# Kernel tuning notes

Hardware: AMD Instinct MI355X
Metric: run time of the kernel (lower is better)

## Reference

```python
import jax, jax.numpy as jnp
import numpy as np

EMBED_DIM = 1024
NUM_HEADS = 16
HEAD_DIM = EMBED_DIM // NUM_HEADS


def setup_inputs() -> dict:
    key = jax.random.key(0)
    ks = jax.random.split(key, 9)
    s = 1.0 / np.sqrt(EMBED_DIM)
    x = jax.random.normal(ks[0], (2, 2048, EMBED_DIM), dtype=jnp.float32)
    # nn.Linear weights are [out, in]; store transposed [in, out] for x @ W
    Wq = jax.random.uniform(ks[1], (EMBED_DIM, EMBED_DIM), jnp.float32, -s, s)
    bq = jax.random.uniform(ks[2], (EMBED_DIM,), jnp.float32, -s, s)
    Wk = jax.random.uniform(ks[3], (EMBED_DIM, EMBED_DIM), jnp.float32, -s, s)
    bk = jax.random.uniform(ks[4], (EMBED_DIM,), jnp.float32, -s, s)
    Wv = jax.random.uniform(ks[5], (EMBED_DIM, EMBED_DIM), jnp.float32, -s, s)
    bv = jax.random.uniform(ks[6], (EMBED_DIM,), jnp.float32, -s, s)
    Wo = jax.random.uniform(ks[7], (EMBED_DIM, EMBED_DIM), jnp.float32, -s, s)
    bo = jax.random.uniform(ks[8], (EMBED_DIM,), jnp.float32, -s, s)
    return {"x": x, "Wq": Wq, "bq": bq, "Wk": Wk, "bk": bk,
            "Wv": Wv, "bv": bv, "Wo": Wo, "bo": bo}


def reference(x, Wq, bq, Wk, bk, Wv, bv, Wo, bo):
    B, N, C = x.shape
    H, D = NUM_HEADS, HEAD_DIM
    scale = 1.0 / np.sqrt(D).astype(np.float32)
    # project and split heads: [B, H, N, D]
    q = (x @ Wq + bq).reshape(B, N, H, D).transpose(0, 2, 1, 3)
    k = (x @ Wk + bk).reshape(B, N, H, D).transpose(0, 2, 1, 3)
    v = (x @ Wv + bv).reshape(B, N, H, D).transpose(0, 2, 1, 3)
    scores = jnp.einsum('bhnd,bhmd->bhnm', q, k) * scale  # [B,H,N,N]
    probs = jax.nn.softmax(scores, axis=-1)
    attn = jnp.einsum('bhnm,bhmd->bhnd', probs, v)  # [B,H,N,D]
    attn = attn.transpose(0, 2, 1, 3).reshape(B, N, C)
    return attn @ Wo + bo
```

## Files before the change

### kernel.cpp

```cpp
#include <hip/hip_runtime.h>
#include <hip/hip_bf16.h>
#include <stdint.h>


#define DEVI __device__ __forceinline__

typedef __attribute__((ext_vector_type(8))) short bf16x8;
typedef __attribute__((ext_vector_type(4))) float f32x4;
typedef __attribute__((ext_vector_type(16))) float f32x16;

#define Z16 ((f32x16){0.f,0.f,0.f,0.f,0.f,0.f,0.f,0.f,0.f,0.f,0.f,0.f,0.f,0.f,0.f,0.f})

DEVI unsigned short f2bf(float f) {
  union { float f; uint32_t u; } v; v.f = f;
  uint32_t u = v.u;
  u += 0x7FFFu + ((u >> 16) & 1u);
  return (unsigned short)(u >> 16);
}

DEVI uint32_t cvtpk_bf16(float lo, float hi) {
  uint32_t r;
  asm("v_cvt_pk_bf16_f32 %0, %1, %2" : "=v"(r) : "v"(lo), "v"(hi));
  return r;
}

DEVI void pl32swap(uint32_t& a, uint32_t& b) {
  asm volatile("v_permlane32_swap_b32 %0, %1" : "+v"(a), "+v"(b));
}

DEVI float fexp2(float x) {
#if __has_builtin(__builtin_amdgcn_exp2f)
  return __builtin_amdgcn_exp2f(x);
#else
  return exp2f(x);
#endif
}

typedef __attribute__((address_space(3))) uint32_t lds_u32_t;
typedef const __attribute__((address_space(1))) uint32_t glb_u32_t;

DEVI void gl2lds16(const void* g, void* l) {
  __builtin_amdgcn_global_load_lds((glb_u32_t*)g, (lds_u32_t*)l, 16, 0, 0);
}

#define MFMA16(a, b, c) __builtin_amdgcn_mfma_f32_16x16x32_bf16((a), (b), (c), 0, 0, 0)
#define MFMA3216(a, b, c) __builtin_amdgcn_mfma_f32_32x32x16_bf16((a), (b), (c), 0, 0, 0)

__global__ void prep_k(const float* __restrict__ x, unsigned short* __restrict__ xb,
                       const float* __restrict__ w0, const float* __restrict__ w1,
                       const float* __restrict__ w2, const float* __restrict__ w3,
                       unsigned short* __restrict__ o0, unsigned short* __restrict__ o1,
                       unsigned short* __restrict__ o2, unsigned short* __restrict__ o3) {
  __shared__ float tile[32][33];
  const int z = blockIdx.z;
  if (z >= 4) {
    int i = ((z - 4) * 1024 + blockIdx.y * 32 + blockIdx.x) * 256 + threadIdx.x;
    float4 a = ((const float4*)x)[i * 2];
    float4 b = ((const float4*)x)[i * 2 + 1];
    union { unsigned short s[8]; uint4 v; } u;
    u.s[0] = f2bf(a.x); u.s[1] = f2bf(a.y); u.s[2] = f2bf(a.z); u.s[3] = f2bf(a.w);
    u.s[4] = f2bf(b.x); u.s[5] = f2bf(b.y); u.s[6] = f2bf(b.z); u.s[7] = f2bf(b.w);
    ((uint4*)xb)[i] = u.v;
    return;
  }
  const float* in = (z == 0) ? w0 : (z == 1) ? w1 : (z == 2) ? w2 : w3;
  unsigned short* out = (z == 0) ? o0 : (z == 1) ? o1 : (z == 2) ? o2 : o3;
  int bx = blockIdx.x * 32, by = blockIdx.y * 32;
  int tx = threadIdx.x & 31, ty = threadIdx.x >> 5;
#pragma unroll
  for (int i = 0; i < 32; i += 8)
    tile[ty + i][tx] = in[(size_t)(by + ty + i) * 1024 + bx + tx];
  __syncthreads();
#pragma unroll
  for (int i = 0; i < 32; i += 8)
    out[(size_t)(bx + ty + i) * 1024 + by + tx] = f2bf(tile[tx][ty + i]);
}

__global__ __launch_bounds__(256, 2)
void gemm_qkv(const unsigned short* __restrict__ A, const unsigned short* __restrict__ Bt,
              const float* __restrict__ bq, const float* __restrict__ bk,
              const float* __restrict__ bv,
              unsigned short* __restrict__ Qb, unsigned short* __restrict__ Kb,
              unsigned short* __restrict__ Vtb) {
  __shared__ unsigned short lA[2][128 * 32];
  __shared__ unsigned short lB[2][128 * 32];
  const int t = threadIdx.x;
  const int mbase = blockIdx.y * 128, nbase = blockIdx.x * 128;
  const int wv = t >> 6, lane = t & 63, lr = lane & 15, lg = lane >> 4;
  const int wr = wv >> 1, wc = wv & 1;
  const int K = 1024;
  const int c0 = t, c1 = t + 256;

#define GSTAGE(buf, k0)                                                                     \
  do {                                                                                      \
    gl2lds16(A + ((size_t)(mbase + (c0 >> 2)) * K + (k0) + (c0 & 3) * 8), &lA[buf][c0 * 8]);\
    gl2lds16(Bt + ((size_t)(nbase + (c0 >> 2)) * K + (k0) + (c0 & 3) * 8), &lB[buf][c0 * 8]);\
    gl2lds16(A + ((size_t)(mbase + (c1 >> 2)) * K + (k0) + (c1 & 3) * 8), &lA[buf][c1 * 8]);\
    gl2lds16(Bt + ((size_t)(nbase + (c1 >> 2)) * K + (k0) + (c1 & 3) * 8), &lB[buf][c1 * 8]);\
  } while (0)

  f32x4 acc[4][4];
#pragma unroll
  for (int i = 0; i < 4; i++)
#pragma unroll
    for (int j = 0; j < 4; j++) acc[i][j] = (f32x4){0.f, 0.f, 0.f, 0.f};

  GSTAGE(0, 0);
  int buf = 0;
  for (int kk = 0; kk < 32; ++kk) {
    if (kk < 31) {
      GSTAGE(buf ^ 1, (kk + 1) * 32);
      asm volatile("s_waitcnt vmcnt(4)");
    } else {
      asm volatile("s_waitcnt vmcnt(0)");
    }
    __builtin_amdgcn_s_barrier();
    __builtin_amdgcn_sched_barrier(0);
    bf16x8 af[4], bfr[4];
#pragma unroll
    for (int i = 0; i < 4; i++)
      af[i] = *(const bf16x8*)&lA[buf][(wr * 64 + i * 16 + lr) * 32 + lg * 8];
#pragma unroll
    for (int j = 0; j < 4; j++)
      bfr[j] = *(const bf16x8*)&lB[buf][(wc * 64 + j * 16 + lr) * 32 + lg * 8];
    __builtin_amdgcn_s_setprio(1);
#pragma unroll
    for (int i = 0; i < 4; i++)
#pragma unroll
      for (int j = 0; j < 4; j++)
        acc[i][j] = MFMA16(af[i], bfr[j], acc[i][j]);
    __builtin_amdgcn_s_setprio(0);
    __builtin_amdgcn_s_barrier();
    buf ^= 1;
  }
#undef GSTAGE

#pragma unroll
  for (int i = 0; i < 4; i++) {
#pragma unroll
    for (int j = 0; j < 4; j++) {
#pragma unroll
      for (int r = 0; r < 4; r++) {
        int grow = mbase + wr * 64 + i * 16 + lg * 4 + r;
        int gcol = nbase + wc * 64 + j * 16 + lr;
        float v = acc[i][j][r];
        if (gcol < 1024) {
          Qb[(size_t)grow * 1024 + gcol] = f2bf((v + bq[gcol]) * 0.18033688011f);
        } else if (gcol < 2048) {
          int c2 = gcol - 1024;
          Kb[(size_t)grow * 1024 + c2] = f2bf(v + bk[c2]);
        } else {
          int vc = gcol - 2048, hh = vc >> 6, d = vc & 63;
          int bb = grow >> 11, np = grow & 2047;
          Vtb[((size_t)((bb * 16 + hh) * 64 + d) << 11) + np] = f2bf(v + bv[vc]);
        }
      }
    }
  }
}

__global__ __launch_bounds__(256, 2)
void gemm_out(const unsigned short* __restrict__ A, const unsigned short* __restrict__ Bt,
              const float* __restrict__ bias, float* __restrict__ outp) {
  __shared__ unsigned short lA[2][128 * 32];
  __shared__ unsigned short lB[2][64 * 32];
  const int t = threadIdx.x;
  const int mbase = blockIdx.y * 128, nbase = blockIdx.x * 64;
  const int wv = t >> 6, lane = t & 63, lr = lane & 15, lg = lane >> 4;
  const int wr = wv >> 1, wc = wv & 1;
  const int K = 1024, N = 1024;
  const int a0 = t, a1 = t + 256;
  const int bg = t;

#define GSTAGE(buf, k0)                                                                     \
  do {                                                                                      \
    gl2lds16(A + ((size_t)(mbase + (a0 >> 2)) * K + (k0) + (a0 & 3) * 8), &lA[buf][a0 * 8]);\
    gl2lds16(A + ((size_t)(mbase + (a1 >> 2)) * K + (k0) + (a1 & 3) * 8), &lA[buf][a1 * 8]);\
    gl2lds16(Bt + ((size_t)(nbase + (bg >> 2)) * K + (k0) + (bg & 3) * 8), &lB[buf][bg * 8]);\
  } while (0)

  f32x4 acc[4][2];
#pragma unroll
  for (int i = 0; i < 4; i++)
#pragma unroll
    for (int j = 0; j < 2; j++) acc[i][j] = (f32x4){0.f, 0.f, 0.f, 0.f};

  GSTAGE(0, 0);
  int buf = 0;
  for (int kk = 0; kk < 32; ++kk) {
    if (kk < 31) {
      GSTAGE(buf ^ 1, (kk + 1) * 32);
      asm volatile("s_waitcnt vmcnt(3)");
    } else {
      asm volatile("s_waitcnt vmcnt(0)");
    }
    __builtin_amdgcn_s_barrier();
    __builtin_amdgcn_sched_barrier(0);
    bf16x8 af[4], bfr[2];
#pragma unroll
    for (int i = 0; i < 4; i++)
      af[i] = *(const bf16x8*)&lA[buf][(wr * 64 + i * 16 + lr) * 32 + lg * 8];
#pragma unroll
    for (int j = 0; j < 2; j++)
      bfr[j] = *(const bf16x8*)&lB[buf][(wc * 32 + j * 16 + lr) * 32 + lg * 8];
    __builtin_amdgcn_s_setprio(1);
#pragma unroll
    for (int i = 0; i < 4; i++)
#pragma unroll
      for (int j = 0; j < 2; j++)
        acc[i][j] = MFMA16(af[i], bfr[j], acc[i][j]);
    __builtin_amdgcn_s_setprio(0);
    __builtin_amdgcn_s_barrier();
    buf ^= 1;
  }
#undef GSTAGE

#pragma unroll
  for (int i = 0; i < 4; i++)
#pragma unroll
    for (int j = 0; j < 2; j++)
#pragma unroll
      for (int r = 0; r < 4; r++) {
        int grow = mbase + wr * 64 + i * 16 + lg * 4 + r;
        int gcol = nbase + wc * 32 + j * 16 + lr;
        outp[(size_t)grow * N + gcol] = acc[i][j][r] + bias[gcol];
      }
}

__global__ __launch_bounds__(256, 2)
void attn_fwd(const unsigned short* __restrict__ Qb, const unsigned short* __restrict__ Kb,
              const unsigned short* __restrict__ Vtb, unsigned short* __restrict__ Ob) {
  const int hb = blockIdx.x, qt = blockIdx.y;
  const int h = hb & 15, b = hb >> 4;
  __shared__ unsigned short lK[2][128 * 64];
  __shared__ unsigned short lV[2][64 * 128];
  const int t = threadIdx.x, wv = t >> 6, lane = t & 63;
  const int q5 = lane & 31, hi = lane >> 5;
  const int sw7 = q5 & 7;
  const int sw15 = q5 & 15;

  const int qrow = b * 2048 + qt * 128 + wv * 32 + q5;
  const size_t qoff = (size_t)qrow * 1024 + h * 64;
  bf16x8 qf[4];
#pragma unroll
  for (int c = 0; c < 4; c++) qf[c] = *(const bf16x8*)&Qb[qoff + c * 16 + hi * 8];

  f32x16 o0 = Z16, o1 = Z16;
  float sum = 0.f;

  const size_t kbase = ((size_t)(b * 2048)) * 1024 + h * 64;
  const size_t vbase = ((size_t)((b * 16 + h) * 64)) * 2048;

#define STAGE(buf, kt)                                                                      \
  do {                                                                                      \
    _Pragma("unroll")                                                                       \
    for (int i = 0; i < 4; i++) {                                                           \
      int c = t + i * 256;                                                                  \
      int rk = c >> 3, sk = ((c & 7) ^ (rk & 7)) * 8;                                       \
      gl2lds16(Kb + kbase + (size_t)((kt) * 128 + rk) * 1024 + sk, &lK[buf][c * 8]);        \
      int rv = c >> 4, sv = ((c & 15) ^ (rv & 15)) * 8;                                     \
      gl2lds16(Vtb + vbase + (size_t)rv * 2048 + (kt) * 128 + sv, &lV[buf][c * 8]);         \
    }                                                                                       \
  } while (0)

  STAGE(0, 0);
  int cur = 0;

  for (int kt = 0; kt < 16; ++kt) {
    if (kt < 15) {
      STAGE(cur ^ 1, kt + 1);
      asm volatile("s_waitcnt vmcnt(8)");
    } else {
      asm volatile("s_waitcnt vmcnt(0)");
    }
    __builtin_amdgcn_s_barrier();
    __builtin_amdgcn_sched_barrier(0);

    const unsigned short* Kc = &lK[cur][0];
    f32x16 s[4];
#pragma unroll
    for (int i = 0; i < 4; i++) s[i] = Z16;
    __builtin_amdgcn_s_setprio(1);
#pragma unroll
    for (int ch = 0; ch < 4; ch++) {
      const int g = ((ch * 2 + hi) ^ sw7) * 8;
#pragma unroll
      for (int sub = 0; sub < 4; sub++) {
        bf16x8 kf = *(const bf16x8*)&Kc[(sub * 32 + q5) * 64 + g];
        s[sub] = MFMA3216(kf, qf[ch], s[sub]);
      }
    }
    __builtin_amdgcn_s_setprio(0);

    const unsigned short* Vc = &lV[cur][0];
    bf16x8 va[8], vb[8];
#pragma unroll
    for (int ck = 0; ck < 8; ck++) {
      const int e = ((ck * 2 + hi) ^ sw15) * 8;
      va[ck] = *(const bf16x8*)&Vc[q5 * 128 + e];
      vb[ck] = *(const bf16x8*)&Vc[(32 + q5) * 128 + e];
    }

    float su0 = 0.f, su1 = 0.f, su2 = 0.f, su3 = 0.f;
#pragma unroll
    for (int i = 0; i < 4; i++) {
#pragma unroll
      for (int r = 0; r < 16; r += 4) {
        s[i][r + 0] = fexp2(s[i][r + 0]); su0 += s[i][r + 0];
        s[i][r + 1] = fexp2(s[i][r + 1]); su1 += s[i][r + 1];
        s[i][r + 2] = fexp2(s[i][r + 2]); su2 += s[i][r + 2];
        s[i][r + 3] = fexp2(s[i][r + 3]); su3 += s[i][r + 3];
      }
    }
    {
      float su = (su0 + su1) + (su2 + su3);
      uint32_t sa = __float_as_uint(su), sb = sa;
      pl32swap(sa, sb);
      sum += __uint_as_float(sa) + __uint_as_float(sb);
    }

    __builtin_amdgcn_s_setprio(1);
#pragma unroll
    for (int ck = 0; ck < 8; ck++) {
      const int base = 8 * (ck & 1);
      const int ti = 2 * (ck >> 2) + ((ck & 3) >> 1);
      uint32_t u0 = cvtpk_bf16(s[ti][base + 0], s[ti][base + 1]);
      uint32_t u1 = cvtpk_bf16(s[ti][base + 2], s[ti][base + 3]);
      uint32_t u2 = cvtpk_bf16(s[ti][base + 4], s[ti][base + 5]);
      uint32_t u3 = cvtpk_bf16(s[ti][base + 6], s[ti][base + 7]);
      pl32swap(u0, u2);
      pl32swap(u1, u3);
      union { uint32_t u[4]; bf16x8 v; } f;
      f.u[0] = u0; f.u[1] = u1; f.u[2] = u2; f.u[3] = u3;
      o0 = MFMA3216(va[ck], f.v, o0);
      o1 = MFMA3216(vb[ck], f.v, o1);
    }
    __builtin_amdgcn_s_setprio(0);
    __builtin_amdgcn_s_barrier();
    cur ^= 1;
  }
#undef STAGE

  float inv = 1.0f / sum;
  const size_t ob = (size_t)qrow * 1024 + h * 64;
#pragma unroll
  for (int a = 0; a < 4; a++) {
    uint2 pk0, pk1;
    pk0.x = cvtpk_bf16(o0[4 * a + 0] * inv, o0[4 * a + 1] * inv);
    pk0.y = cvtpk_bf16(o0[4 * a + 2] * inv, o0[4 * a + 3] * inv);
    *(uint2*)&Ob[ob + 8 * a + 4 * hi] = pk0;
    pk1.x = cvtpk_bf16(o1[4 * a + 0] * inv, o1[4 * a + 1] * inv);
    pk1.y = cvtpk_bf16(o1[4 * a + 2] * inv, o1[4 * a + 3] * inv);
    *(uint2*)&Ob[ob + 32 + 8 * a + 4 * hi] = pk1;
  }
}

extern "C" void kernel_launch(void* const* d_in, const int* in_sizes, int n_in,
                              void* d_out, int out_size, void* d_ws, size_t ws_size,
                              hipStream_t stream) {
  const float* x  = (const float*)d_in[0];
  const float* Wq = (const float*)d_in[1];
  const float* bq = (const float*)d_in[2];
  const float* Wk = (const float*)d_in[3];
  const float* bk = (const float*)d_in[4];
  const float* Wv = (const float*)d_in[5];
  const float* bv = (const float*)d_in[6];
  const float* Wo = (const float*)d_in[7];
  const float* bo = (const float*)d_in[8];
  float* out = (float*)d_out;

  char* ws = (char*)d_ws;
  const size_t MB = 1024u * 1024u;
  unsigned short* xb    = (unsigned short*)(ws + 0);
  unsigned short* wqkvt = (unsigned short*)(ws + 8 * MB);
  unsigned short* wot   = (unsigned short*)(ws + 14 * MB);
  unsigned short* Qb    = (unsigned short*)(ws + 16 * MB);
  unsigned short* Kb    = (unsigned short*)(ws + 24 * MB);
  unsigned short* Vtb   = (unsigned short*)(ws + 32 * MB);
  unsigned short* Ab    = (unsigned short*)(ws + 40 * MB);

  prep_k<<<dim3(32, 32, 6), 256, 0, stream>>>(
      x, xb, Wq, Wk, Wv, Wo, wqkvt, wqkvt + 1024 * 1024, wqkvt + 2048 * 1024, wot);
  gemm_qkv<<<dim3(24, 32), 256, 0, stream>>>(xb, wqkvt, bq, bk, bv, Qb, Kb, Vtb);
  attn_fwd<<<dim3(32, 16), 256, 0, stream>>>(Qb, Kb, Vtb, Ab);
  gemm_out<<<dim3(16, 32), 256, 0, stream>>>(Ab, wot, bo, out);
}
```

Measured before the change: 118.1 us.

## Double QKV GEMM K-tile to 64 and XOR-swizzle LDS layout

The QKV projection GEMM now stages 64-wide K slices instead of 32, halving the number of main-loop iterations and the barriers between them. The LDS layout is XOR-swizzled by row so the 16-byte fragment reads avoid bank conflicts. LDS use doubles to 64 KB per block, which may limit how many blocks fit per CU under the launch bound of two. Register pressure also rises from holding twice the fragments.

```diff
diff --git a/kernel.cpp b/kernel.cpp
--- a/kernel.cpp
+++ b/kernel.cpp
@@ -82,21 +82,23 @@
               const float* __restrict__ bv,
               unsigned short* __restrict__ Qb, unsigned short* __restrict__ Kb,
               unsigned short* __restrict__ Vtb) {
-  __shared__ unsigned short lA[2][128 * 32];
-  __shared__ unsigned short lB[2][128 * 32];
+  __shared__ unsigned short lA[2][128 * 64];
+  __shared__ unsigned short lB[2][128 * 64];
   const int t = threadIdx.x;
   const int mbase = blockIdx.y * 128, nbase = blockIdx.x * 128;
   const int wv = t >> 6, lane = t & 63, lr = lane & 15, lg = lane >> 4;
   const int wr = wv >> 1, wc = wv & 1;
   const int K = 1024;
-  const int c0 = t, c1 = t + 256;
 
 #define GSTAGE(buf, k0)                                                                     \
   do {                                                                                      \
-    gl2lds16(A + ((size_t)(mbase + (c0 >> 2)) * K + (k0) + (c0 & 3) * 8), &lA[buf][c0 * 8]);\
-    gl2lds16(Bt + ((size_t)(nbase + (c0 >> 2)) * K + (k0) + (c0 & 3) * 8), &lB[buf][c0 * 8]);\
-    gl2lds16(A + ((size_t)(mbase + (c1 >> 2)) * K + (k0) + (c1 & 3) * 8), &lA[buf][c1 * 8]);\
-    gl2lds16(Bt + ((size_t)(nbase + (c1 >> 2)) * K + (k0) + (c1 & 3) * 8), &lB[buf][c1 * 8]);\
+    _Pragma("unroll")                                                                       \
+    for (int i = 0; i < 4; i++) {                                                           \
+      int g = t + i * 256;                                                                  \
+      int row = g >> 3, kg = ((g & 7) ^ (row & 7)) * 8;                                     \
+      gl2lds16(A + ((size_t)(mbase + row) * K + (k0) + kg), &lA[buf][g * 8]);               \
+      gl2lds16(Bt + ((size_t)(nbase + row) * K + (k0) + kg), &lB[buf][g * 8]);              \
+    }                                                                                       \
   } while (0)
 
   f32x4 acc[4][4];
@@ -107,28 +109,37 @@
 
   GSTAGE(0, 0);
   int buf = 0;
-  for (int kk = 0; kk < 32; ++kk) {
-    if (kk < 31) {
-      GSTAGE(buf ^ 1, (kk + 1) * 32);
-      asm volatile("s_waitcnt vmcnt(4)");
+  const int cs0 = ((0 * 4 + lg) ^ (lr & 7)) * 8;
+  const int cs1 = ((1 * 4 + lg) ^ (lr & 7)) * 8;
+
+  for (int kk = 0; kk < 16; ++kk) {
+    if (kk < 15) {
+      GSTAGE(buf ^ 1, (kk + 1) * 64);
+      asm volatile("s_waitcnt vmcnt(8)");
     } else {
       asm volatile("s_waitcnt vmcnt(0)");
     }
     __builtin_amdgcn_s_barrier();
     __builtin_amdgcn_sched_barrier(0);
-    bf16x8 af[4], bfr[4];
+    bf16x8 af[4][2], bfr[4][2];
+#pragma unroll
+    for (int i = 0; i < 4; i++) {
+      af[i][0] = *(const bf16x8*)&lA[buf][(wr * 64 + i * 16 + lr) * 64 + cs0];
+      af[i][1] = *(const bf16x8*)&lA[buf][(wr * 64 + i * 16 + lr) * 64 + cs1];
+    }
+#pragma unroll
+    for (int j = 0; j < 4; j++) {
+      bfr[j][0] = *(const bf16x8*)&lB[buf][(wc * 64 + j * 16 + lr) * 64 + cs0];
+      bfr[j][1] = *(const bf16x8*)&lB[buf][(wc * 64 + j * 16 + lr) * 64 + cs1];
+    }
+    __builtin_amdgcn_s_setprio(1);
 #pragma unroll
     for (int i = 0; i < 4; i++)
-      af[i] = *(const bf16x8*)&lA[buf][(wr * 64 + i * 16 + lr) * 32 + lg * 8];
-#pragma unroll
-    for (int j = 0; j < 4; j++)
-      bfr[j] = *(const bf16x8*)&lB[buf][(wc * 64 + j * 16 + lr) * 32 + lg * 8];
-    __builtin_amdgcn_s_setprio(1);
-#pragma unroll
-    for (int i = 0; i < 4; i++)
-#pragma unroll
-      for (int j = 0; j < 4; j++)
-        acc[i][j] = MFMA16(af[i], bfr[j], acc[i][j]);
+#pragma unroll
+      for (int j = 0; j < 4; j++) {
+        acc[i][j] = MFMA16(af[i][0], bfr[j][0], acc[i][j]);
+        acc[i][j] = MFMA16(af[i][1], bfr[j][1], acc[i][j]);
+      }
     __builtin_amdgcn_s_setprio(0);
     __builtin_amdgcn_s_barrier();
     buf ^= 1;
```

Measured after the change: 137.5 us. 16.4% more time.

## Single-buffer V tile in LDS and stage it after PV with split waits

Applied to the files above, without the earlier changes.

Reduces LDS use by single-buffering the V tile. V for the next iteration is issued after the PV MFMA barrier, while K stays double-buffered. A second wait plus barrier is inserted before V reads, so the V load overlaps only the QK^T phase of the next iteration. This aims to raise occupancy by cutting shared memory, at the cost of an extra barrier and less prefetch distance for V. The vmcnt(8) wait at the top now also waits on the previous V loads, which changes the ordering semantics.

```diff
diff --git a/kernel.cpp b/kernel.cpp
--- a/kernel.cpp
+++ b/kernel.cpp
@@ -233,7 +233,7 @@
   const int hb = blockIdx.x, qt = blockIdx.y;
   const int h = hb & 15, b = hb >> 4;
   __shared__ unsigned short lK[2][128 * 64];
-  __shared__ unsigned short lV[2][64 * 128];
+  __shared__ unsigned short lV[64 * 128];
   const int t = threadIdx.x, wv = t >> 6, lane = t & 63;
   const int q5 = lane & 31, hi = lane >> 5;
   const int sw7 = q5 & 7;
@@ -251,24 +251,32 @@
   const size_t kbase = ((size_t)(b * 2048)) * 1024 + h * 64;
   const size_t vbase = ((size_t)((b * 16 + h) * 64)) * 2048;
 
-#define STAGE(buf, kt)                                                                      \
+#define STAGE_K(buf, kt)                                                                    \
   do {                                                                                      \
     _Pragma("unroll")                                                                       \
     for (int i = 0; i < 4; i++) {                                                           \
       int c = t + i * 256;                                                                  \
       int rk = c >> 3, sk = ((c & 7) ^ (rk & 7)) * 8;                                       \
       gl2lds16(Kb + kbase + (size_t)((kt) * 128 + rk) * 1024 + sk, &lK[buf][c * 8]);        \
-      int rv = c >> 4, sv = ((c & 15) ^ (rv & 15)) * 8;                                     \
-      gl2lds16(Vtb + vbase + (size_t)rv * 2048 + (kt) * 128 + sv, &lV[buf][c * 8]);         \
     }                                                                                       \
   } while (0)
-
-  STAGE(0, 0);
+#define STAGE_V(kt)                                                                         \
+  do {                                                                                      \
+    _Pragma("unroll")                                                                       \
+    for (int i = 0; i < 4; i++) {                                                           \
+      int c = t + i * 256;                                                                  \
+      int rv = c >> 4, sv = ((c & 15) ^ (rv & 15)) * 8;                                     \
+      gl2lds16(Vtb + vbase + (size_t)rv * 2048 + (kt) * 128 + sv, &lV[c * 8]);              \
+    }                                                                                       \
+  } while (0)
+
+  STAGE_K(0, 0);
+  STAGE_V(0);
   int cur = 0;
 
   for (int kt = 0; kt < 16; ++kt) {
     if (kt < 15) {
-      STAGE(cur ^ 1, kt + 1);
+      STAGE_K(cur ^ 1, kt + 1);
       asm volatile("s_waitcnt vmcnt(8)");
     } else {
       asm volatile("s_waitcnt vmcnt(0)");
@@ -292,13 +300,20 @@
     }
     __builtin_amdgcn_s_setprio(0);
 
-    const unsigned short* Vc = &lV[cur][0];
+    if (kt < 15) {
+      asm volatile("s_waitcnt vmcnt(4)");
+    } else {
+      asm volatile("s_waitcnt vmcnt(0)");
+    }
+    __builtin_amdgcn_s_barrier();
+    __builtin_amdgcn_sched_barrier(0);
+
     bf16x8 va[8], vb[8];
 #pragma unroll
     for (int ck = 0; ck < 8; ck++) {
       const int e = ((ck * 2 + hi) ^ sw15) * 8;
-      va[ck] = *(const bf16x8*)&Vc[q5 * 128 + e];
-      vb[ck] = *(const bf16x8*)&Vc[(32 + q5) * 128 + e];
+      va[ck] = *(const bf16x8*)&lV[q5 * 128 + e];
+      vb[ck] = *(const bf16x8*)&lV[(32 + q5) * 128 + e];
     }
 
     float su0 = 0.f, su1 = 0.f, su2 = 0.f, su3 = 0.f;
@@ -337,9 +352,11 @@
     }
     __builtin_amdgcn_s_setprio(0);
     __builtin_amdgcn_s_barrier();
+    if (kt < 15) STAGE_V(kt + 1);
     cur ^= 1;
   }
-#undef STAGE
+#undef STAGE_K
+#undef STAGE_V
 
   float inv = 1.0f / sum;
   const size_t ob = (size_t)qrow * 1024 + h * 64;
```

Result: no change. 119.1 us (+0.8%).

## Restructure QKV GEMM into 256x256 tiles with swizzled LDS and phased pipelining

Applied to the files above, without the earlier changes.

The QKV projection GEMM moves from 128x128 tiles with 4 waves to 256x256 tiles with 8 waves and a K-step of 64. LDS loads use an XOR swizzle to avoid bank conflicts, and each K-step is split into four quadrant phases that interleave global-to-LDS prefetch with MFMA work. Blocks are remapped across XCDs for L2 locality, and the launch becomes 192 blocks. The larger tiles raise data reuse and cut global traffic, but only 192 blocks are launched and LDS use per block goes up, which can limit occupancy and tail balance.

```diff
diff --git a/kernel.cpp b/kernel.cpp
--- a/kernel.cpp
+++ b/kernel.cpp
@@ -76,77 +76,115 @@
     out[(size_t)(bx + ty + i) * 1024 + by + tx] = f2bf(tile[tx][ty + i]);
 }
 
-__global__ __launch_bounds__(256, 2)
+__global__ __launch_bounds__(512, 2)
 void gemm_qkv(const unsigned short* __restrict__ A, const unsigned short* __restrict__ Bt,
               const float* __restrict__ bq, const float* __restrict__ bk,
               const float* __restrict__ bv,
               unsigned short* __restrict__ Qb, unsigned short* __restrict__ Kb,
               unsigned short* __restrict__ Vtb) {
-  __shared__ unsigned short lA[2][128 * 32];
-  __shared__ unsigned short lB[2][128 * 32];
+  __shared__ unsigned short lA[2][2][128 * 64];
+  __shared__ unsigned short lB[2][2][128 * 64];
   const int t = threadIdx.x;
-  const int mbase = blockIdx.y * 128, nbase = blockIdx.x * 128;
-  const int wv = t >> 6, lane = t & 63, lr = lane & 15, lg = lane >> 4;
-  const int wr = wv >> 1, wc = wv & 1;
-  const int K = 1024;
-  const int c0 = t, c1 = t + 256;
-
-#define GSTAGE(buf, k0)                                                                     \
-  do {                                                                                      \
-    gl2lds16(A + ((size_t)(mbase + (c0 >> 2)) * K + (k0) + (c0 & 3) * 8), &lA[buf][c0 * 8]);\
-    gl2lds16(Bt + ((size_t)(nbase + (c0 >> 2)) * K + (k0) + (c0 & 3) * 8), &lB[buf][c0 * 8]);\
-    gl2lds16(A + ((size_t)(mbase + (c1 >> 2)) * K + (k0) + (c1 & 3) * 8), &lA[buf][c1 * 8]);\
-    gl2lds16(Bt + ((size_t)(nbase + (c1 >> 2)) * K + (k0) + (c1 & 3) * 8), &lB[buf][c1 * 8]);\
+  const int wid = t >> 6, lane = t & 63, lr = lane & 15, lg = lane >> 4;
+  const int wr = wid >> 2, wc = wid & 3;
+  const int xcd = blockIdx.x & 7, idx = blockIdx.x >> 3;
+  const int by = (xcd >> 1) * 4 + idx / 6;
+  const int bx = (xcd & 1) * 6 + idx % 6;
+  const int mbase = by * 256, nbase = bx * 256;
+
+  const int g0 = t, g1 = t + 512;
+  const int R0 = g0 >> 3, R1 = g1 >> 3;
+  const int kg0 = ((g0 & 7) ^ (R0 & 7)) * 8, kg1 = ((g1 & 7) ^ (R1 & 7)) * 8;
+  const int arow0 = (R0 >> 6) * 128 + (R0 & 63), arow1 = (R1 >> 6) * 128 + (R1 & 63);
+  const int brow0 = (R0 >> 5) * 64 + (R0 & 31), brow1 = (R1 >> 5) * 64 + (R1 & 31);
+
+#define STG_A(bf, mh, kt) do { \
+    gl2lds16(A + (size_t)(mbase + (mh) * 64 + arow0) * 1024 + (kt) * 64 + kg0, &lA[bf][mh][g0 * 8]); \
+    gl2lds16(A + (size_t)(mbase + (mh) * 64 + arow1) * 1024 + (kt) * 64 + kg1, &lA[bf][mh][g1 * 8]); \
   } while (0)
-
-  f32x4 acc[4][4];
-#pragma unroll
-  for (int i = 0; i < 4; i++)
+#define STG_B(bf, nh, kt) do { \
+    gl2lds16(Bt + (size_t)(nbase + (nh) * 32 + brow0) * 1024 + (kt) * 64 + kg0, &lB[bf][nh][g0 * 8]); \
+    gl2lds16(Bt + (size_t)(nbase + (nh) * 32 + brow1) * 1024 + (kt) * 64 + kg1, &lB[bf][nh][g1 * 8]); \
+  } while (0)
+
+  f32x4 acc[8][4];
+#pragma unroll
+  for (int i = 0; i < 8; i++)
 #pragma unroll
     for (int j = 0; j < 4; j++) acc[i][j] = (f32x4){0.f, 0.f, 0.f, 0.f};
 
-  GSTAGE(0, 0);
-  int buf = 0;
-  for (int kk = 0; kk < 32; ++kk) {
-    if (kk < 31) {
-      GSTAGE(buf ^ 1, (kk + 1) * 32);
-      asm volatile("s_waitcnt vmcnt(4)");
-    } else {
-      asm volatile("s_waitcnt vmcnt(0)");
-    }
-    __builtin_amdgcn_s_barrier();
-    __builtin_amdgcn_sched_barrier(0);
-    bf16x8 af[4], bfr[4];
-#pragma unroll
-    for (int i = 0; i < 4; i++)
-      af[i] = *(const bf16x8*)&lA[buf][(wr * 64 + i * 16 + lr) * 32 + lg * 8];
-#pragma unroll
-    for (int j = 0; j < 4; j++)
-      bfr[j] = *(const bf16x8*)&lB[buf][(wc * 64 + j * 16 + lr) * 32 + lg * 8];
-    __builtin_amdgcn_s_setprio(1);
-#pragma unroll
-    for (int i = 0; i < 4; i++)
-#pragma unroll
-      for (int j = 0; j < 4; j++)
-        acc[i][j] = MFMA16(af[i], bfr[j], acc[i][j]);
-    __builtin_amdgcn_s_setprio(0);
-    __builtin_amdgcn_s_barrier();
-    buf ^= 1;
-  }
-#undef GSTAGE
-
-#pragma unroll
-  for (int i = 0; i < 4; i++) {
+  const int cs0 = (lg ^ (lr & 7)) * 8;
+  const int cs1 = ((4 + lg) ^ (lr & 7)) * 8;
+
+  STG_A(0, 0, 0); STG_B(0, 0, 0); STG_B(0, 1, 0); STG_A(0, 1, 0);
+  asm volatile("s_waitcnt vmcnt(4)");
+  __builtin_amdgcn_s_barrier();
+
+#define PHASE(bf, MH, NH, STG_STMT, VM_STMT) do {                                \
+    const unsigned short* Ah = &lA[bf][MH][0];                                   \
+    const unsigned short* Bh = &lB[bf][NH][0];                                   \
+    bf16x8 a0_[4], a1_[4], b0_[2], b1_[2];                                       \
+    _Pragma("unroll")                                                            \
+    for (int mq = 0; mq < 4; mq++) {                                             \
+      const int ro = (wr * 64 + mq * 16 + lr) * 64;                              \
+      a0_[mq] = *(const bf16x8*)&Ah[ro + cs0];                                   \
+      a1_[mq] = *(const bf16x8*)&Ah[ro + cs1];                                   \
+    }                                                                            \
+    _Pragma("unroll")                                                            \
+    for (int nq = 0; nq < 2; nq++) {                                             \
+      const int ro = (wc * 32 + nq * 16 + lr) * 64;                              \
+      b0_[nq] = *(const bf16x8*)&Bh[ro + cs0];                                   \
+      b1_[nq] = *(const bf16x8*)&Bh[ro + cs1];                                   \
+    }                                                                            \
+    STG_STMT;                                                                    \
+    VM_STMT;                                                                     \
+    asm volatile("s_waitcnt lgkmcnt(8)");                                        \
+    __builtin_amdgcn_s_barrier();                                                \
+    asm volatile("s_waitcnt lgkmcnt(0)");                                        \
+    __builtin_amdgcn_s_setprio(1);                                               \
+    _Pragma("unroll")                                                            \
+    for (int mq = 0; mq < 4; mq++)                                               \
+      _Pragma("unroll")                                                          \
+      for (int nq = 0; nq < 2; nq++) {                                           \
+        acc[(MH) * 4 + mq][(NH) * 2 + nq] =                                      \
+            MFMA16(a0_[mq], b0_[nq], acc[(MH) * 4 + mq][(NH) * 2 + nq]);         \
+        acc[(MH) * 4 + mq][(NH) * 2 + nq] =                                      \
+            MFMA16(a1_[mq], b1_[nq], acc[(MH) * 4 + mq][(NH) * 2 + nq]);         \
+      }                                                                          \
+    __builtin_amdgcn_s_setprio(0);                                               \
+    __builtin_amdgcn_s_barrier();                                                \
+  } while (0)
+
+  for (int kt = 0; kt < 16; ++kt) {
+    const int bf = kt & 1, nb = bf ^ 1;
+    const bool pf = (kt < 15);
+    PHASE(bf, 0, 0, { if (pf) STG_A(nb, 0, kt + 1); },
+          { if (pf) { asm volatile("s_waitcnt vmcnt(4)"); }
+            else    { asm volatile("s_waitcnt vmcnt(2)"); } });
+    PHASE(bf, 0, 1, { if (pf) STG_B(nb, 0, kt + 1); },
+          { if (pf) { asm volatile("s_waitcnt vmcnt(4)"); }
+            else    { asm volatile("s_waitcnt vmcnt(0)"); } });
+    PHASE(bf, 1, 0, { if (pf) STG_B(nb, 1, kt + 1); }, {});
+    PHASE(bf, 1, 1, { if (pf) STG_A(nb, 1, kt + 1); },
+          { if (pf) { asm volatile("s_waitcnt vmcnt(4)"); } });
+  }
+#undef PHASE
+#undef STG_A
+#undef STG_B
+
+  const int region = bx >> 2;
+#pragma unroll
+  for (int i = 0; i < 8; i++) {
 #pragma unroll
     for (int j = 0; j < 4; j++) {
 #pragma unroll
       for (int r = 0; r < 4; r++) {
-        int grow = mbase + wr * 64 + i * 16 + lg * 4 + r;
-        int gcol = nbase + wc * 64 + j * 16 + lr;
+        int grow = mbase + wr * 128 + (i >> 2) * 64 + (i & 3) * 16 + lg * 4 + r;
+        int gcol = nbase + wc * 64 + (j >> 1) * 32 + (j & 1) * 16 + lr;
         float v = acc[i][j][r];
-        if (gcol < 1024) {
+        if (region == 0) {
           Qb[(size_t)grow * 1024 + gcol] = f2bf((v + bq[gcol]) * 0.18033688011f);
-        } else if (gcol < 2048) {
+        } else if (region == 1) {
           int c2 = gcol - 1024;
           Kb[(size_t)grow * 1024 + c2] = f2bf(v + bk[c2]);
         } else {
@@ -381,7 +419,7 @@
 
   prep_k<<<dim3(32, 32, 6), 256, 0, stream>>>(
       x, xb, Wq, Wk, Wv, Wo, wqkvt, wqkvt + 1024 * 1024, wqkvt + 2048 * 1024, wot);
-  gemm_qkv<<<dim3(24, 32), 256, 0, stream>>>(xb, wqkvt, bq, bk, bv, Qb, Kb, Vtb);
+  gemm_qkv<<<192, 512, 0, stream>>>(xb, wqkvt, bq, bk, bv, Qb, Kb, Vtb);
   attn_fwd<<<dim3(32, 16), 256, 0, stream>>>(Qb, Kb, Vtb, Ab);
   gemm_out<<<dim3(16, 32), 256, 0, stream>>>(Ab, wot, bo, out);
 }
```

After: 148.7 us. 25.9% more time.
